# Performance work log

Hardware: AMD Instinct MI355X
Metric: run time of the kernel (lower is better)

## Reference

```python
import jax, jax.numpy as jnp
import numpy as np

BN_EPS = 1e-5

def _bn(x, gamma, beta, relu=True):
    # training-mode BatchNorm over all dims except channel (last)
    axes = tuple(range(x.ndim - 1))
    mu = jnp.mean(x, axes, keepdims=True)
    var = jnp.var(x, axes, keepdims=True)
    y = (x - mu) / jnp.sqrt(var + BN_EPS) * gamma + beta
    return jax.nn.relu(y) if relu else y

def _l2norm(x, eps):
    # F.normalize: x / max(||x||, eps)
    n = jnp.sqrt(jnp.sum(x * x, axis=-1, keepdims=True))
    return x / jnp.maximum(n, eps)

def setup_inputs() -> dict:
    key = jax.random.key(0)
    ks = jax.random.split(key, 16)
    B, N, H, W, C = 2, 512, 16, 32, 64
    IN_DIM = 10 + C + C + 2  # 140
    MLP3 = [128, 64]
    s = 0.02
    inp = {
        "warped_xyz": jax.random.normal(ks[0], (B, N, 3), jnp.float32),
        "warped_points": jax.random.normal(ks[1], (B, N, C), jnp.float32),
        "RF3": jax.random.normal(ks[2], (B, C, H, W), jnp.float32),
        "RF3_index": jax.random.normal(ks[3], (B, 3, H, W), jnp.float32),
        "lidar_z": jax.random.uniform(ks[4], (B, N, 1), jnp.float32),
        # conv1x1 stack (mlp3)
        "W1": jax.random.normal(ks[5], (IN_DIM, MLP3[0]), jnp.float32) * s,
        "b1": jnp.zeros((MLP3[0],), jnp.float32),
        "g1": jnp.ones((MLP3[0],), jnp.float32),
        "be1": jnp.zeros((MLP3[0],), jnp.float32),
        "W2": jax.random.normal(ks[6], (MLP3[0], MLP3[1]), jnp.float32) * s,
        "b2": jnp.zeros((MLP3[1],), jnp.float32),
        "g2": jnp.ones((MLP3[1],), jnp.float32),
        "be2": jnp.zeros((MLP3[1],), jnp.float32),
        # conv1d stack (mlp4 = [feats_dim//2], then 2 logits)
        "M1w": jax.random.normal(ks[7], (MLP3[1], MLP3[1] // 2), jnp.float32) * s,
        "M1b": jnp.zeros((MLP3[1] // 2,), jnp.float32),
        "M1g": jnp.ones((MLP3[1] // 2,), jnp.float32),
        "M1be": jnp.zeros((MLP3[1] // 2,), jnp.float32),
        "M2w": jax.random.normal(ks[8], (MLP3[1] // 2, 2), jnp.float32) * s,
        "M2b": jnp.zeros((2,), jnp.float32),
    }
    return inp

def reference(warped_xyz, warped_points, RF3, RF3_index, lidar_z,
              W1, b1, g1, be1, W2, b2, g2, be2,
              M1w, M1b, M1g, M1be, M2w, M2b):
    B, N, _ = warped_xyz.shape
    _, Ci, H, W_ = RF3.shape
    M = H * W_
    RF3_bnc = RF3.transpose(0, 2, 3, 1).reshape(B, M, Ci)          # [B,M,C]
    idx_bnc = RF3_index.transpose(0, 2, 3, 1).reshape(B, M, 3)     # [B,M,3]

    src_xyz = warped_xyz[:, :, None, :]                             # [B,N,1,3]
    dst_xyz = idx_bnc[:, None, :, :]                                # [B,1,M,3]
    euc = (src_xyz - dst_xyz)[..., :2]                              # [B,N,M,2]
    euc_norm = jnp.sqrt(euc[..., 0:1] ** 2 + euc[..., 1:2] ** 2)    # [B,N,M,1]

    xyz_z = (warped_xyz * lidar_z)[:, :, None, :]                   # [B,N,1,3]
    src_pts = warped_points[:, :, None, :]                          # [B,N,1,C]
    dst_pts = RF3_bnc[:, None, :, :]                                # [B,1,M,C]

    geom = jnp.concatenate([
        jnp.broadcast_to(xyz_z, (B, N, M, 3)),
        jnp.broadcast_to(src_pts[..., :2], (B, N, M, 2)),
        jnp.broadcast_to(dst_xyz[..., :2], (B, N, M, 2)),
        euc, euc_norm], axis=-1)                                    # [B,N,M,10]
    desc = jnp.concatenate([
        jnp.broadcast_to(src_pts, (B, N, M, Ci)),
        jnp.broadcast_to(dst_pts, (B, N, M, Ci))], axis=-1)         # [B,N,M,2C]

    # cal_sim: cosine sim between lidar feats (src) and image feats (dst)
    src_n = _l2norm(warped_points, 1e-12)
    dst_n = _l2norm(RF3_bnc, 1e-12)
    cos = jnp.einsum('bnc,bmc->bnm', src_n, dst_n)                  # [B,N,M]
    s1 = cos / (jnp.max(cos, axis=2, keepdims=True) + 1e-6)         # src->dst norm
    s2 = cos / (jnp.max(cos, axis=1, keepdims=True) + 1e-10)        # dst->src norm
    sim = jnp.stack([s1, s2], axis=-1)                              # [B,N,M,2]

    feats = jnp.concatenate([geom, desc, sim], axis=-1)             # [B,N,M,140]
    feats = _bn(jnp.einsum('bnmi,io->bnmo', feats, W1) + b1, g1, be1)
    feats = _bn(jnp.einsum('bnmi,io->bnmo', feats, W2) + b2, g2, be2)

    aw = jax.nn.softmax(jnp.max(feats, axis=-1), axis=-1)           # [B,N,M]
    att = jnp.einsum('bnm,bnmc->bnc', aw, feats)                    # [B,N,C]

    att = _bn(att @ M1w + M1b, M1g, M1be)
    logits = att @ M2w + M2b                                        # [B,N,2]
    return logits
```

## Files before the change

### kernel.cpp

```cpp
#include <hip/hip_runtime.h>
#include <hip/hip_bf16.h>

#define B_ 2
#define N_ 512
#define M_ 512
#define C_ 64
#define O1 128
#define O2 64
#define O3 32
#define PBIG 524288.0f
#define P3   1024.0f

typedef short s8v __attribute__((ext_vector_type(8)));
typedef float f4v __attribute__((ext_vector_type(4)));

#define WS_SRCN 0
#define WS_DSTN 65536
#define WS_P0   0
#define WS_U    131072
#define WS_Z    131072
#define WS_V    262144
#define WS_DXY  393216
#define WS_COS  395264
#define WS_RMAX 919552
#define WS_ST1  920576
#define WS_ST2  936960
#define WS_ST3  945152
#define WS_CMAX 949248
#define WS_W2F  950272
#define WS_W9S  954368
#define WS_X2   961536

__device__ __forceinline__ unsigned short f2bf(float f){
  unsigned u = __float_as_uint(f);
  unsigned r = (u + 0x7fffu + ((u >> 16) & 1u)) >> 16;
  return (unsigned short)r;
}
__device__ __forceinline__ float bf2f(unsigned short h){
  return __uint_as_float(((unsigned)h) << 16);
}
__device__ __forceinline__ unsigned pk_trunc(float lo, float hi){
  return __builtin_amdgcn_perm(__float_as_uint(hi), __float_as_uint(lo), 0x07060302u);
}
__device__ __forceinline__ f4v relu4(f4v z){
  z[0] = fmaxf(z[0], 0.f); z[1] = fmaxf(z[1], 0.f);
  z[2] = fmaxf(z[2], 0.f); z[3] = fmaxf(z[3], 0.f);
  return z;
}

__global__ __launch_bounds__(128) void k1(const float* __restrict__ wxyz,
    const float* __restrict__ wpts, const float* __restrict__ lz,
    const float* __restrict__ rf3, const float* __restrict__ rf3i,
    const float* __restrict__ W1, float* __restrict__ ws){
  int t = threadIdx.x;
  if (blockIdx.x < 1024){
    int blk = blockIdx.x; int b = blk >> 9, n = blk & 511;
    int bn = b*N_ + n;
    __shared__ float wp[64]; __shared__ float sxyz[3]; __shared__ float slz; __shared__ float srn;
    if (t < 64) wp[t] = wpts[bn*64 + t];
    if (t >= 64 && t < 67) sxyz[t-64] = wxyz[bn*3 + (t-64)];
    if (t == 67) slz = lz[bn];
    __syncthreads();
    if (t < 64){
      float v = wp[t]*wp[t];
      v += __shfl_down(v,32); v += __shfl_down(v,16); v += __shfl_down(v,8);
      v += __shfl_down(v,4);  v += __shfl_down(v,2);  v += __shfl_down(v,1);
      if (t == 0) srn = 1.0f / fmaxf(sqrtf(v), 1e-12f);
    }
    __syncthreads();
    if (t < 64) ws[WS_SRCN + bn*64 + t] = wp[t]*srn;
    int o = t;
    float x = sxyz[0], y = sxyz[1], z = sxyz[2], l = slz;
    float acc = x*l*W1[0*O1+o] + y*l*W1[1*O1+o] + z*l*W1[2*O1+o]
              + wp[0]*W1[3*O1+o] + wp[1]*W1[4*O1+o]
              + x*W1[7*O1+o] + y*W1[8*O1+o];
    #pragma unroll 8
    for (int c = 0; c < 64; ++c) acc += wp[c]*W1[(10+c)*O1+o];
    ws[WS_U + bn*O1 + o] = acc;
  } else {
    int blk = blockIdx.x - 1024; int b = blk >> 9, m = blk & 511;
    int bm = b*M_ + m;
    __shared__ float rf[64]; __shared__ float sdx, sdy, srn2;
    if (t < 64) rf[t] = rf3[(b*64 + t)*512 + m];
    if (t == 64) sdx = rf3i[(b*3 + 0)*512 + m];
    if (t == 65) sdy = rf3i[(b*3 + 1)*512 + m];
    __syncthreads();
    if (t < 64){
      float v = rf[t]*rf[t];
      v += __shfl_down(v,32); v += __shfl_down(v,16); v += __shfl_down(v,8);
      v += __shfl_down(v,4);  v += __shfl_down(v,2);  v += __shfl_down(v,1);
      if (t == 0) srn2 = 1.0f / fmaxf(sqrtf(v), 1e-12f);
    }
    __syncthreads();
    if (t < 64) ws[WS_DSTN + bm*64 + t] = rf[t]*srn2;
    if (t == 0){ ws[WS_DXY + bm*2+0] = sdx; ws[WS_DXY + bm*2+1] = sdy; }
    int o = t;
    float acc = sdx*(W1[5*O1+o] - W1[7*O1+o]) + sdy*(W1[6*O1+o] - W1[8*O1+o]);
    #pragma unroll 8
    for (int c = 0; c < 64; ++c) acc += rf[c]*W1[(74+c)*O1+o];
    ws[WS_V + bm*O1 + o] = acc;
  }
}

__global__ __launch_bounds__(256) void k2(float* __restrict__ ws){
  int blk = blockIdx.x; int b = blk >> 9, n = blk & 511; int t = threadIdx.x;
  int bn = b*N_ + n;
  __shared__ __align__(16) float sn[64];
  __shared__ float dnt[64*65];
  __shared__ float part[4*64];
  if (t < 64) sn[t] = ws[WS_SRCN + bn*64 + t];
  float lmax = -3.4e38f;
  for (int chunk = 0; chunk < 8; ++chunk){
    __syncthreads();
    const float4* src = (const float4*)(ws + WS_DSTN + (size_t)(b*M_ + chunk*64)*64);
    #pragma unroll
    for (int i = 0; i < 4; ++i){
      float4 v = src[t + i*256];
      int base = (t + i*256)*4; int mm = base >> 6, c = base & 63;
      float* dp = &dnt[mm*65 + c];
      dp[0]=v.x; dp[1]=v.y; dp[2]=v.z; dp[3]=v.w;
    }
    __syncthreads();
    {
      int mm = t & 63, cg = t >> 6;
      const float* dr = &dnt[mm*65 + cg*16];
      const float* sr = &sn[cg*16];
      float p = 0.f;
      #pragma unroll
      for (int k = 0; k < 16; ++k) p += sr[k]*dr[k];
      part[cg*64 + mm] = p;
    }
    __syncthreads();
    if (t < 64){
      float d = part[t] + part[64+t] + part[128+t] + part[192+t];
      ws[WS_COS + bn*M_ + chunk*64 + t] = d;
      lmax = fmaxf(lmax, d);
    }
  }
  if (t < 64){
    lmax = fmaxf(lmax, __shfl_xor(lmax,32)); lmax = fmaxf(lmax, __shfl_xor(lmax,16));
    lmax = fmaxf(lmax, __shfl_xor(lmax,8));  lmax = fmaxf(lmax, __shfl_xor(lmax,4));
    lmax = fmaxf(lmax, __shfl_xor(lmax,2));  lmax = fmaxf(lmax, __shfl_xor(lmax,1));
    if (t == 0) ws[WS_RMAX + bn] = 1.0f / (lmax + 1e-6f);
  }
}

__global__ __launch_bounds__(256) void k2r(float* __restrict__ ws){
  int blk = blockIdx.x;
  int b = blk >> 4; int c0 = (blk & 15)*32;
  int t = threadIdx.x;
  int col = c0 + (t & 31), seg = t >> 5;
  float mx = -3.4e38f;
  #pragma unroll 8
  for (int i = 0; i < 64; ++i){
    int n = seg*64 + i;
    mx = fmaxf(mx, ws[WS_COS + (size_t)(b*N_ + n)*M_ + col]);
  }
  __shared__ float sred[256];
  sred[t] = mx;
  __syncthreads();
  if (t < 32){
    float m2 = sred[t];
    #pragma unroll
    for (int s2 = 1; s2 < 8; ++s2) m2 = fmaxf(m2, sred[s2*32 + t]);
    ws[WS_CMAX + b*M_ + c0 + t] = 1.0f / (m2 + 1e-10f);
  }
}

__global__ __launch_bounds__(256) void k3(const float* __restrict__ wxyz,
    const float* __restrict__ W1, const float* __restrict__ b1, float* __restrict__ ws){
  int blk = blockIdx.x; int bn = blk >> 1, half = blk & 1; int t = threadIdx.x;
  int b = bn >> 9; int mbase = half*256;
  __shared__ float s_en[256], s_s1[256], s_s2[256];
  __shared__ float sred[512];
  float sx = wxyz[bn*3+0], sy = wxyz[bn*3+1];
  float ri = ws[WS_RMAX + bn];
  {
    int m = mbase + t;
    float2 d = *(const float2*)(ws + WS_DXY + (size_t)(b*M_+m)*2);
    float ex = sx-d.x, ey = sy-d.y;
    s_en[t] = sqrtf(ex*ex + ey*ey);
    float cv = ws[WS_COS + (size_t)bn*M_ + m];
    s_s1[t] = cv*ri;
    s_s2[t] = cv*ws[WS_CMAX + b*M_ + m];
  }
  __syncthreads();
  int o = t & 127, mh = t >> 7;
  float u  = ws[WS_U + bn*O1 + o] + b1[o];
  float w9 = W1[9*O1+o], wa = W1[138*O1+o], wb = W1[139*O1+o];
  float sum = 0.f, ssq = 0.f;
  const float* Vp = ws + WS_V + (size_t)b*M_*O1 + o;
  int lBeg = mh*128, lEnd = lBeg + 128;
  #pragma unroll 8
  for (int ml = lBeg; ml < lEnd; ++ml){
    float xv = u + Vp[(size_t)(mbase+ml)*O1] + s_en[ml]*w9 + s_s1[ml]*wa + s_s2[ml]*wb;
    sum += xv; ssq += xv*xv;
  }
  sred[mh*128 + o] = sum;
  sred[256 + mh*128 + o] = ssq;
  __syncthreads();
  if (t < 128){
    float S = sred[t] + sred[128+t];
    float Q = sred[256+t] + sred[384+t];
    int rep = blk & 63;
    atomicAdd(&ws[WS_ST1 + rep*256 + t], S);
    atomicAdd(&ws[WS_ST1 + rep*256 + 128 + t], Q);
  }
}

__global__ __launch_bounds__(128) void k3b(const float* __restrict__ W1,
    const float* __restrict__ b1, const float* __restrict__ g1,
    const float* __restrict__ be1, const float* __restrict__ W2, float* __restrict__ ws){
  int blk = blockIdx.x; int t = threadIdx.x;
  int o = t;
  float s = 0.f, q = 0.f;
  #pragma unroll 8
  for (int r = 0; r < 64; ++r){ s += ws[WS_ST1 + r*256 + o]; q += ws[WS_ST1 + r*256 + 128 + o]; }
  float mu = s/PBIG, var = q/PBIG - mu*mu;
  float istd = rsqrtf(var + 1e-5f);
  float A1 = g1[o]*istd, C1 = be1[o] - mu*A1;
  if (blk < 1024){
    int bn = blk;
    ws[WS_P0 + bn*O1 + o] = (ws[WS_U + bn*O1 + o] + b1[o])*A1 + C1;
  } else if (blk < 1040){
    int r0 = (blk - 1024)*64;
    for (int r = 0; r < 64; ++r)
      ws[WS_V + (size_t)(r0 + r)*O1 + o] *= A1;
  } else {
    ws[WS_W9S + o]       = W1[9*O1+o]*A1;
    ws[WS_W9S + 128 + o] = W1[138*O1+o]*A1;
    ws[WS_W9S + 256 + o] = W1[139*O1+o]*A1;
    unsigned short* wf = (unsigned short*)(ws + WS_W2F);
    for (int i = t; i < 8192; i += 128){
      int j = i & 7, ll = (i >> 3) & 63, ct = (i >> 9) & 3, k0q = i >> 11;
      int oo = k0q*32 + (ll >> 4)*8 + j, c = ct*16 + (ll & 15);
      wf[i] = f2bf(W2[oo*O2 + c]);
    }
  }
}

__global__ __launch_bounds__(256, 4) void k4(const float* __restrict__ wxyz,
    float* __restrict__ ws){
  int bn = blockIdx.x; int b = bn >> 9; int t = threadIdx.x;
  __shared__ __align__(16) unsigned short wBf[8192];
  __shared__ __align__(16) float p0s[128], w9s[128], was[128], wbs[128];
  __shared__ float ls[64], lq[64];
  {
    const s8v* g = (const s8v*)(ws + WS_W2F);
    s8v* l = (s8v*)wBf;
    #pragma unroll
    for (int c2 = 0; c2 < 4; ++c2) l[c2*256 + t] = g[c2*256 + t];
  }
  if (t < 64){ ls[t] = 0.f; lq[t] = 0.f; }
  if (t < 128){
    p0s[t] = ws[WS_P0 + bn*O1 + t];
    w9s[t] = ws[WS_W9S + t];
    was[t] = ws[WS_W9S + 128 + t];
    wbs[t] = ws[WS_W9S + 256 + t];
  }
  __syncthreads();
  int ll = t & 63, w = t >> 6, l16 = ll & 15, quad = ll >> 4;
  float sx = wxyz[bn*3+0], sy = wxyz[bn*3+1];
  float ri = ws[WS_RMAX + bn];
  float sst[4][4], sq2[4][4];
  #pragma unroll
  for (int i = 0; i < 4; ++i)
    #pragma unroll
    for (int j = 0; j < 4; ++j){ sst[i][j] = 0.f; sq2[i][j] = 0.f; }
  uint2* xf = (uint2*)(ws + WS_X2) + (size_t)bn*8192;
  union U8 { s8v v; unsigned u[4]; };
  #pragma unroll
  for (int mc = 0; mc < 4; ++mc){
    int mA = mc*128 + w*32 + l16, mB = mA + 16;
    float2 dA = *(const float2*)(ws + WS_DXY + (size_t)(b*M_+mA)*2);
    float2 dB = *(const float2*)(ws + WS_DXY + (size_t)(b*M_+mB)*2);
    float cvA = ws[WS_COS + (size_t)bn*M_ + mA], cvB = ws[WS_COS + (size_t)bn*M_ + mB];
    float ciA = ws[WS_CMAX + b*M_ + mA],         ciB = ws[WS_CMAX + b*M_ + mB];
    float exA = sx-dA.x, eyA = sy-dA.y; float en0 = sqrtf(exA*exA + eyA*eyA);
    float exB = sx-dB.x, eyB = sy-dB.y; float en1 = sqrtf(exB*exB + eyB*eyB);
    float s10 = cvA*ri, s20 = cvA*ciA;
    float s11 = cvB*ri, s21 = cvB*ciB;
    const float* vpA = ws + WS_V + (size_t)(b*M_+mA)*O1;
    const float* vpB = ws + WS_V + (size_t)(b*M_+mB)*O1;
    f4v acc[2][4];
    #pragma unroll
    for (int i = 0; i < 2; ++i)
      #pragma unroll
      for (int j = 0; j < 4; ++j) acc[i][j] = (f4v){0.f,0.f,0.f,0.f};
    #pragma unroll
    for (int k0q = 0; k0q < 4; ++k0q){
      int ko = k0q*32 + quad*8;
      f4v p0a = *(const f4v*)&p0s[ko], p0b = *(const f4v*)&p0s[ko+4];
      f4v w9a = *(const f4v*)&w9s[ko], w9b = *(const f4v*)&w9s[ko+4];
      f4v waa = *(const f4v*)&was[ko], wab = *(const f4v*)&was[ko+4];
      f4v wba = *(const f4v*)&wbs[ko], wbb = *(const f4v*)&wbs[ko+4];
      f4v vA0 = *(const f4v*)(vpA + ko), vA1 = *(const f4v*)(vpA + ko + 4);
      f4v vB0 = *(const f4v*)(vpB + ko), vB1 = *(const f4v*)(vpB + ko + 4);
      f4v zaA = relu4(p0a + vA0 + en0*w9a + s10*waa + s20*wba);
      f4v zbA = relu4(p0b + vA1 + en0*w9b + s10*wab + s20*wbb);
      f4v zaB = relu4(p0a + vB0 + en1*w9a + s11*waa + s21*wba);
      f4v zbB = relu4(p0b + vB1 + en1*w9b + s11*wab + s21*wbb);
      U8 uA, uB;
      uA.u[0] = pk_trunc(zaA[0], zaA[1]); uA.u[1] = pk_trunc(zaA[2], zaA[3]);
      uA.u[2] = pk_trunc(zbA[0], zbA[1]); uA.u[3] = pk_trunc(zbA[2], zbA[3]);
      uB.u[0] = pk_trunc(zaB[0], zaB[1]); uB.u[1] = pk_trunc(zaB[2], zaB[3]);
      uB.u[2] = pk_trunc(zbB[0], zbB[1]); uB.u[3] = pk_trunc(zbB[2], zbB[3]);
      #pragma unroll
      for (int ct = 0; ct < 4; ++ct){
        s8v bb = *(const s8v*)&wBf[((k0q*4 + ct)*64 + ll)*8];
        acc[0][ct] = __builtin_amdgcn_mfma_f32_16x16x32_bf16(bb, uA.v, acc[0][ct], 0,0,0);
        acc[1][ct] = __builtin_amdgcn_mfma_f32_16x16x32_bf16(bb, uB.v, acc[1][ct], 0,0,0);
      }
    }
    #pragma unroll
    for (int ct = 0; ct < 4; ++ct){
      #pragma unroll
      for (int mt = 0; mt < 2; ++mt){
        uint2 uv;
        uv.x = (unsigned)f2bf(acc[mt][ct][0]) | ((unsigned)f2bf(acc[mt][ct][1]) << 16);
        uv.y = (unsigned)f2bf(acc[mt][ct][2]) | ((unsigned)f2bf(acc[mt][ct][3]) << 16);
        xf[(((mc*4 + w)*4 + ct)*2 + mt)*64 + ll] = uv;
      }
      #pragma unroll
      for (int r = 0; r < 4; ++r){
        float a0 = acc[0][ct][r], a1 = acc[1][ct][r];
        sst[ct][r] += a0 + a1;
        sq2[ct][r] += a0*a0 + a1*a1;
      }
    }
  }
  #pragma unroll
  for (int ct = 0; ct < 4; ++ct){
    #pragma unroll
    for (int r = 0; r < 4; ++r){
      float s = sst[ct][r], q = sq2[ct][r];
      s += __shfl_xor(s,1); s += __shfl_xor(s,2); s += __shfl_xor(s,4); s += __shfl_xor(s,8);
      q += __shfl_xor(q,1); q += __shfl_xor(q,2); q += __shfl_xor(q,4); q += __shfl_xor(q,8);
      if (l16 == 0){
        atomicAdd(&ls[ct*16 + quad*4 + r], s);
        atomicAdd(&lq[ct*16 + quad*4 + r], q);
      }
    }
  }
  __syncthreads();
  int rep = bn & 63;
  if (t < 64) atomicAdd(&ws[WS_ST2 + rep*128 + t], ls[t]);
  else if (t < 128) atomicAdd(&ws[WS_ST2 + rep*128 + t], lq[t-64]);
}

__global__ __launch_bounds__(256) void k5(const float* __restrict__ g2,
    const float* __restrict__ be2, const float* __restrict__ M1w,
    const float* __restrict__ M1b, float* __restrict__ ws){
  int bn = blockIdx.x; int t = threadIdx.x;
  __shared__ float sa2[64], sc2[64];
  __shared__ float s_mx[512];
  __shared__ float s_aw[512];
  __shared__ float red[256];
  __shared__ float part[64*65];
  __shared__ float s_att[64];
  __shared__ float sgmax, sinvS;
  if (t < 64){
    float s = 0.f, q = 0.f;
    #pragma unroll 8
    for (int r = 0; r < 64; ++r){ s += ws[WS_ST2 + r*128 + t]; q += ws[WS_ST2 + r*128 + 64 + t]; }
    float mu = s/PBIG, var = q/PBIG - mu*mu;
    float istd = rsqrtf(var + 1e-5f);
    float A2 = g2[t]*istd;
    sa2[t] = A2; sc2[t] = be2[t] - mu*A2;
  }
  __syncthreads();
  int ll = t & 63, w = t >> 6, l16 = ll & 15, quad = ll >> 4;
  const uint2* xf = (const uint2*)(ws + WS_X2) + (size_t)bn*8192;
  uint2 xv[4][4][2];
  #pragma unroll
  for (int mc = 0; mc < 4; ++mc)
    #pragma unroll
    for (int ct = 0; ct < 4; ++ct)
      #pragma unroll
      for (int mt = 0; mt < 2; ++mt)
        xv[mc][ct][mt] = xf[(((mc*4 + w)*4 + ct)*2 + mt)*64 + ll];
  float a2r[4][4], c2r[4][4];
  #pragma unroll
  for (int ct = 0; ct < 4; ++ct)
    #pragma unroll
    for (int r = 0; r < 4; ++r){
      int c = ct*16 + quad*4 + r;
      a2r[ct][r] = sa2[c]; c2r[ct][r] = sc2[c];
    }
  #pragma unroll
  for (int mc = 0; mc < 4; ++mc){
    #pragma unroll
    for (int mt = 0; mt < 2; ++mt){
      float mx = 0.f;
      #pragma unroll
      for (int ct = 0; ct < 4; ++ct){
        uint2 uv = xv[mc][ct][mt];
        float x0 = bf2f((unsigned short)(uv.x & 0xffffu));
        float x1 = bf2f((unsigned short)(uv.x >> 16));
        float x2 = bf2f((unsigned short)(uv.y & 0xffffu));
        float x3 = bf2f((unsigned short)(uv.y >> 16));
        mx = fmaxf(mx, a2r[ct][0]*x0 + c2r[ct][0]);
        mx = fmaxf(mx, a2r[ct][1]*x1 + c2r[ct][1]);
        mx = fmaxf(mx, a2r[ct][2]*x2 + c2r[ct][2]);
        mx = fmaxf(mx, a2r[ct][3]*x3 + c2r[ct][3]);
      }
      mx = fmaxf(mx, __shfl_xor(mx,16));
      mx = fmaxf(mx, __shfl_xor(mx,32));
      if (quad == 0) s_mx[mc*128 + w*32 + mt*16 + l16] = mx;
    }
  }
  __syncthreads();
  red[t] = fmaxf(s_mx[t], s_mx[t+256]);
  __syncthreads();
  for (int s = 128; s > 0; s >>= 1){ if (t < s) red[t] = fmaxf(red[t], red[t+s]); __syncthreads(); }
  if (t == 0) sgmax = red[0];
  __syncthreads();
  float e0 = expf(s_mx[t] - sgmax), e1 = expf(s_mx[t+256] - sgmax);
  s_aw[t] = e0; s_aw[t+256] = e1;
  red[t] = e0 + e1;
  __syncthreads();
  for (int s = 128; s > 0; s >>= 1){ if (t < s) red[t] += red[t+s]; __syncthreads(); }
  if (t == 0) sinvS = 1.0f / red[0];
  __syncthreads();
  float acc[4][4];
  #pragma unroll
  for (int ct = 0; ct < 4; ++ct)
    #pragma unroll
    for (int r = 0; r < 4; ++r) acc[ct][r] = 0.f;
  #pragma unroll
  for (int mc = 0; mc < 4; ++mc){
    #pragma unroll
    for (int mt = 0; mt < 2; ++mt){
      float aw = s_aw[mc*128 + w*32 + mt*16 + l16];
      #pragma unroll
      for (int ct = 0; ct < 4; ++ct){
        uint2 uv = xv[mc][ct][mt];
        float x0 = bf2f((unsigned short)(uv.x & 0xffffu));
        float x1 = bf2f((unsigned short)(uv.x >> 16));
        float x2 = bf2f((unsigned short)(uv.y & 0xffffu));
        float x3 = bf2f((unsigned short)(uv.y >> 16));
        acc[ct][0] += aw*fmaxf(a2r[ct][0]*x0 + c2r[ct][0], 0.f);
        acc[ct][1] += aw*fmaxf(a2r[ct][1]*x1 + c2r[ct][1], 0.f);
        acc[ct][2] += aw*fmaxf(a2r[ct][2]*x2 + c2r[ct][2], 0.f);
        acc[ct][3] += aw*fmaxf(a2r[ct][3]*x3 + c2r[ct][3], 0.f);
      }
    }
  }
  int row = w*16 + l16;
  #pragma unroll
  for (int ct = 0; ct < 4; ++ct)
    #pragma unroll
    for (int r = 0; r < 4; ++r)
      part[row*65 + ct*16 + quad*4 + r] = acc[ct][r];
  __syncthreads();
  if (t < 64){
    float a = 0.f;
    #pragma unroll 8
    for (int r = 0; r < 64; ++r) a += part[r*65 + t];
    s_att[t] = a * sinvS;
  }
  __syncthreads();
  if (t < 32){
    float z = M1b[t];
    #pragma unroll 8
    for (int c = 0; c < 64; ++c) z += s_att[c]*M1w[c*32 + t];
    ws[WS_Z + bn*32 + t] = z;
    int rep = bn & 63;
    atomicAdd(&ws[WS_ST3 + rep*64 + t], z);
    atomicAdd(&ws[WS_ST3 + rep*64 + 32 + t], z*z);
  }
}

__global__ __launch_bounds__(256) void k6(const float* __restrict__ M1g,
    const float* __restrict__ M1be, const float* __restrict__ M2w,
    const float* __restrict__ M2b, const float* __restrict__ ws, float* __restrict__ out){
  int t = threadIdx.x; int s = blockIdx.x*256 + t;
  __shared__ float sa3[32], sc3[32];
  if (t < 32){
    float su = 0.f, q = 0.f;
    #pragma unroll 8
    for (int r = 0; r < 64; ++r){ su += ws[WS_ST3 + r*64 + t]; q += ws[WS_ST3 + r*64 + 32 + t]; }
    float mu = su/P3, var = q/P3 - mu*mu;
    float istd = rsqrtf(var + 1e-5f);
    float A3 = M1g[t]*istd;
    sa3[t] = A3; sc3[t] = M1be[t] - mu*A3;
  }
  __syncthreads();
  float a0 = M2b[0], a1 = M2b[1];
  #pragma unroll
  for (int j = 0; j < 32; ++j){
    float y = fmaxf(ws[WS_Z + s*32 + j]*sa3[j] + sc3[j], 0.f);
    a0 += y*M2w[j*2+0]; a1 += y*M2w[j*2+1];
  }
  out[s*2+0] = a0; out[s*2+1] = a1;
}

extern "C" void kernel_launch(void* const* d_in, const int* in_sizes, int n_in,
                              void* d_out, int out_size, void* d_ws, size_t ws_size,
                              hipStream_t stream){
  const float* wxyz = (const float*)d_in[0];
  const float* wpts = (const float*)d_in[1];
  const float* rf3  = (const float*)d_in[2];
  const float* rf3i = (const float*)d_in[3];
  const float* lz   = (const float*)d_in[4];
  const float* W1   = (const float*)d_in[5];
  const float* b1   = (const float*)d_in[6];
  const float* g1   = (const float*)d_in[7];
  const float* be1  = (const float*)d_in[8];
  const float* W2   = (const float*)d_in[9];
  const float* g2   = (const float*)d_in[11];
  const float* be2  = (const float*)d_in[12];
  const float* M1w  = (const float*)d_in[13];
  const float* M1b  = (const float*)d_in[14];
  const float* M1g  = (const float*)d_in[15];
  const float* M1be = (const float*)d_in[16];
  const float* M2w  = (const float*)d_in[17];
  const float* M2b  = (const float*)d_in[18];
  float* ws  = (float*)d_ws;
  float* out = (float*)d_out;
  hipMemsetAsync(ws + WS_ST1, 0, 28672*sizeof(float), stream);
  k1 <<<2048,128,0,stream>>>(wxyz, wpts, lz, rf3, rf3i, W1, ws);
  k2 <<<1024,256,0,stream>>>(ws);
  k2r<<<32,256,0,stream>>>(ws);
  k3 <<<2048,256,0,stream>>>(wxyz, W1, b1, ws);
  k3b<<<1041,128,0,stream>>>(W1, b1, g1, be1, W2, ws);
  k4 <<<1024,256,0,stream>>>(wxyz, ws);
  k5 <<<1024,256,0,stream>>>(g2, be2, M1w, M1b, ws);
  k6 <<<4,256,0,stream>>>(M1g, M1be, M2w, M2b, ws, out);
}
```

Measured before the change: 250.3 us.

## Split k4 per point across two blocks and widen intermediate stores to 128-bit

k4 now launches two blocks per (b,n) point, each handling half of the M range, with launch bounds raised to allow 8 blocks per CU. This raises parallelism and occupancy for the MFMA-heavy second layer. The bf16 intermediate buffer is repacked so each lane writes and reads uint4 (two channel tiles) instead of uint2, with k5's loads and unpacking adjusted to match. In exchange, each block reloads the 16 KB weight tile into LDS, the stats atomics double, and the tighter register budget may cause spills.

```diff
diff --git a/kernel.cpp b/kernel.cpp
--- a/kernel.cpp
+++ b/kernel.cpp
@@ -38,6 +38,9 @@
 }
 __device__ __forceinline__ float bf2f(unsigned short h){
   return __uint_as_float(((unsigned)h) << 16);
+}
+__device__ __forceinline__ unsigned pk2(float lo, float hi){
+  return (unsigned)f2bf(lo) | ((unsigned)f2bf(hi) << 16);
 }
 __device__ __forceinline__ unsigned pk_trunc(float lo, float hi){
   return __builtin_amdgcn_perm(__float_as_uint(hi), __float_as_uint(lo), 0x07060302u);
@@ -239,9 +242,10 @@
   }
 }
 
-__global__ __launch_bounds__(256, 4) void k4(const float* __restrict__ wxyz,
+__global__ __launch_bounds__(256, 8) void k4(const float* __restrict__ wxyz,
     float* __restrict__ ws){
-  int bn = blockIdx.x; int b = bn >> 9; int t = threadIdx.x;
+  int blk = blockIdx.x; int bn = blk >> 1, half = blk & 1;
+  int b = bn >> 9; int t = threadIdx.x;
   __shared__ __align__(16) unsigned short wBf[8192];
   __shared__ __align__(16) float p0s[128], w9s[128], was[128], wbs[128];
   __shared__ float ls[64], lq[64];
@@ -267,10 +271,11 @@
   for (int i = 0; i < 4; ++i)
     #pragma unroll
     for (int j = 0; j < 4; ++j){ sst[i][j] = 0.f; sq2[i][j] = 0.f; }
-  uint2* xf = (uint2*)(ws + WS_X2) + (size_t)bn*8192;
+  uint4* xf4 = (uint4*)(ws + WS_X2) + (size_t)bn*4096;
   union U8 { s8v v; unsigned u[4]; };
   #pragma unroll
-  for (int mc = 0; mc < 4; ++mc){
+  for (int mci = 0; mci < 2; ++mci){
+    int mc = half*2 + mci;
     int mA = mc*128 + w*32 + l16, mB = mA + 16;
     float2 dA = *(const float2*)(ws + WS_DXY + (size_t)(b*M_+mA)*2);
     float2 dB = *(const float2*)(ws + WS_DXY + (size_t)(b*M_+mB)*2);
@@ -313,21 +318,23 @@
       }
     }
     #pragma unroll
-    for (int ct = 0; ct < 4; ++ct){
-      #pragma unroll
-      for (int mt = 0; mt < 2; ++mt){
-        uint2 uv;
-        uv.x = (unsigned)f2bf(acc[mt][ct][0]) | ((unsigned)f2bf(acc[mt][ct][1]) << 16);
-        uv.y = (unsigned)f2bf(acc[mt][ct][2]) | ((unsigned)f2bf(acc[mt][ct][3]) << 16);
-        xf[(((mc*4 + w)*4 + ct)*2 + mt)*64 + ll] = uv;
-      }
+    for (int mt = 0; mt < 2; ++mt){
+      uint4 u0, u1;
+      u0.x = pk2(acc[mt][0][0], acc[mt][0][1]); u0.y = pk2(acc[mt][0][2], acc[mt][0][3]);
+      u0.z = pk2(acc[mt][1][0], acc[mt][1][1]); u0.w = pk2(acc[mt][1][2], acc[mt][1][3]);
+      u1.x = pk2(acc[mt][2][0], acc[mt][2][1]); u1.y = pk2(acc[mt][2][2], acc[mt][2][3]);
+      u1.z = pk2(acc[mt][3][0], acc[mt][3][1]); u1.w = pk2(acc[mt][3][2], acc[mt][3][3]);
+      xf4[((((mc*4 + w)*2 + mt)*2 + 0)*64) + ll] = u0;
+      xf4[((((mc*4 + w)*2 + mt)*2 + 1)*64) + ll] = u1;
+    }
+    #pragma unroll
+    for (int ct = 0; ct < 4; ++ct)
       #pragma unroll
       for (int r = 0; r < 4; ++r){
         float a0 = acc[0][ct][r], a1 = acc[1][ct][r];
         sst[ct][r] += a0 + a1;
         sq2[ct][r] += a0*a0 + a1*a1;
       }
-    }
   }
   #pragma unroll
   for (int ct = 0; ct < 4; ++ct){
@@ -343,7 +350,7 @@
     }
   }
   __syncthreads();
-  int rep = bn & 63;
+  int rep = blk & 63;
   if (t < 64) atomicAdd(&ws[WS_ST2 + rep*128 + t], ls[t]);
   else if (t < 128) atomicAdd(&ws[WS_ST2 + rep*128 + t], lq[t-64]);
 }
@@ -370,15 +377,15 @@
   }
   __syncthreads();
   int ll = t & 63, w = t >> 6, l16 = ll & 15, quad = ll >> 4;
-  const uint2* xf = (const uint2*)(ws + WS_X2) + (size_t)bn*8192;
-  uint2 xv[4][4][2];
+  const uint4* xf4 = (const uint4*)(ws + WS_X2) + (size_t)bn*4096;
+  uint4 xv[4][2][2];
   #pragma unroll
   for (int mc = 0; mc < 4; ++mc)
     #pragma unroll
-    for (int ct = 0; ct < 4; ++ct)
-      #pragma unroll
-      for (int mt = 0; mt < 2; ++mt)
-        xv[mc][ct][mt] = xf[(((mc*4 + w)*4 + ct)*2 + mt)*64 + ll];
+    for (int mt = 0; mt < 2; ++mt)
+      #pragma unroll
+      for (int cp = 0; cp < 2; ++cp)
+        xv[mc][mt][cp] = xf4[((((mc*4 + w)*2 + mt)*2 + cp)*64) + ll];
   float a2r[4][4], c2r[4][4];
   #pragma unroll
   for (int ct = 0; ct < 4; ++ct)
@@ -393,16 +400,25 @@
     for (int mt = 0; mt < 2; ++mt){
       float mx = 0.f;
       #pragma unroll
-      for (int ct = 0; ct < 4; ++ct){
-        uint2 uv = xv[mc][ct][mt];
+      for (int cp = 0; cp < 2; ++cp){
+        uint4 uv = xv[mc][mt][cp];
+        int c0t = 2*cp, c1t = 2*cp + 1;
         float x0 = bf2f((unsigned short)(uv.x & 0xffffu));
         float x1 = bf2f((unsigned short)(uv.x >> 16));
         float x2 = bf2f((unsigned short)(uv.y & 0xffffu));
         float x3 = bf2f((unsigned short)(uv.y >> 16));
-        mx = fmaxf(mx, a2r[ct][0]*x0 + c2r[ct][0]);
-        mx = fmaxf(mx, a2r[ct][1]*x1 + c2r[ct][1]);
-        mx = fmaxf(mx, a2r[ct][2]*x2 + c2r[ct][2]);
-        mx = fmaxf(mx, a2r[ct][3]*x3 + c2r[ct][3]);
+        float x4 = bf2f((unsigned short)(uv.z & 0xffffu));
+        float x5 = bf2f((unsigned short)(uv.z >> 16));
+        float x6 = bf2f((unsigned short)(uv.w & 0xffffu));
+        float x7 = bf2f((unsigned short)(uv.w >> 16));
+        mx = fmaxf(mx, a2r[c0t][0]*x0 + c2r[c0t][0]);
+        mx = fmaxf(mx, a2r[c0t][1]*x1 + c2r[c0t][1]);
+        mx = fmaxf(mx, a2r[c0t][2]*x2 + c2r[c0t][2]);
+        mx = fmaxf(mx, a2r[c0t][3]*x3 + c2r[c0t][3]);
+        mx = fmaxf(mx, a2r[c1t][0]*x4 + c2r[c1t][0]);
+        mx = fmaxf(mx, a2r[c1t][1]*x5 + c2r[c1t][1]);
+        mx = fmaxf(mx, a2r[c1t][2]*x6 + c2r[c1t][2]);
+        mx = fmaxf(mx, a2r[c1t][3]*x7 + c2r[c1t][3]);
       }
       mx = fmaxf(mx, __shfl_xor(mx,16));
       mx = fmaxf(mx, __shfl_xor(mx,32));
@@ -433,16 +449,25 @@
     for (int mt = 0; mt < 2; ++mt){
       float aw = s_aw[mc*128 + w*32 + mt*16 + l16];
       #pragma unroll
-      for (int ct = 0; ct < 4; ++ct){
-        uint2 uv = xv[mc][ct][mt];
+      for (int cp = 0; cp < 2; ++cp){
+        uint4 uv = xv[mc][mt][cp];
+        int c0t = 2*cp, c1t = 2*cp + 1;
         float x0 = bf2f((unsigned short)(uv.x & 0xffffu));
         float x1 = bf2f((unsigned short)(uv.x >> 16));
         float x2 = bf2f((unsigned short)(uv.y & 0xffffu));
         float x3 = bf2f((unsigned short)(uv.y >> 16));
-        acc[ct][0] += aw*fmaxf(a2r[ct][0]*x0 + c2r[ct][0], 0.f);
-        acc[ct][1] += aw*fmaxf(a2r[ct][1]*x1 + c2r[ct][1], 0.f);
-        acc[ct][2] += aw*fmaxf(a2r[ct][2]*x2 + c2r[ct][2], 0.f);
-        acc[ct][3] += aw*fmaxf(a2r[ct][3]*x3 + c2r[ct][3], 0.f);
+        float x4 = bf2f((unsigned short)(uv.z & 0xffffu));
+        float x5 = bf2f((unsigned short)(uv.z >> 16));
+        float x6 = bf2f((unsigned short)(uv.w & 0xffffu));
+        float x7 = bf2f((unsigned short)(uv.w >> 16));
+        acc[c0t][0] += aw*fmaxf(a2r[c0t][0]*x0 + c2r[c0t][0], 0.f);
+        acc[c0t][1] += aw*fmaxf(a2r[c0t][1]*x1 + c2r[c0t][1], 0.f);
+        acc[c0t][2] += aw*fmaxf(a2r[c0t][2]*x2 + c2r[c0t][2], 0.f);
+        acc[c0t][3] += aw*fmaxf(a2r[c0t][3]*x3 + c2r[c0t][3], 0.f);
+        acc[c1t][0] += aw*fmaxf(a2r[c1t][0]*x4 + c2r[c1t][0], 0.f);
+        acc[c1t][1] += aw*fmaxf(a2r[c1t][1]*x5 + c2r[c1t][1], 0.f);
+        acc[c1t][2] += aw*fmaxf(a2r[c1t][2]*x6 + c2r[c1t][2], 0.f);
+        acc[c1t][3] += aw*fmaxf(a2r[c1t][3]*x7 + c2r[c1t][3], 0.f);
       }
     }
   }
@@ -524,7 +549,7 @@
   k2r<<<32,256,0,stream>>>(ws);
   k3 <<<2048,256,0,stream>>>(wxyz, W1, b1, ws);
   k3b<<<1041,128,0,stream>>>(W1, b1, g1, be1, W2, ws);
-  k4 <<<1024,256,0,stream>>>(wxyz, ws);
+  k4 <<<2048,256,0,stream>>>(wxyz, ws);
   k5 <<<1024,256,0,stream>>>(g2, be2, M1w, M1b, ws);
   k6 <<<4,256,0,stream>>>(M1g, M1be, M2w, M2b, ws, out);
 }
```

After: 310.3 us. 23.9% more time.
